# Optimization experiments

Measured on AMD Instinct MI355X. Metric: run time of the kernel, lower is better.

Reference implementation:

```python
import jax, jax.numpy as jnp
import numpy as np

SMALL_CONST = 1e-8
K = 128
N = 512 * 512  # pixels


def setup_inputs() -> dict:
    key = jax.random.key(0)
    ks = jax.random.split(key, 6)
    pos = jax.random.uniform(ks[0], (N, 2), jnp.float32, 0.0, 512.0)      # pixel coords
    mu = jax.random.uniform(ks[1], (K, 2), jnp.float32, 0.0, 512.0)       # gaussian centers
    alpha = jax.random.uniform(ks[2], (K,), jnp.float32)                   # opacities in [0,1]
    color = jax.random.uniform(ks[3], (K, 3), jnp.float32, 0.0, 255.0)     # RGB in [0,255]
    scales = 10.0 + jax.random.uniform(ks[4], (K, 2), jnp.float32) * 20.0  # anisotropic scales
    thetas = jax.random.uniform(ks[5], (K,), jnp.float32, -np.pi, np.pi)   # rotations
    return dict(pos=pos, mu=mu, alpha=alpha, color=color, scales=scales, thetas=thetas)


def _forward(pos, mu, alpha, color, scales, thetas):
    # Parameter clamps done at the top of the torch forward
    alpha = jnp.clip(alpha, 0.0, 1.0)
    color = jnp.clip(color, 0.0, 255.0)
    scales = jnp.clip(scales, 0.1, None)

    # Precompute all K inverse covariances: sigma_inv = R diag(1/s^2) R^T  -> [K,2,2]
    c, s = jnp.cos(thetas), jnp.sin(thetas)
    R = jnp.stack([jnp.stack([c, -s], -1), jnp.stack([s, c], -1)], -2)  # [K,2,2]
    inv2 = 1.0 / scales ** 2                                            # [K,2]
    sigma_inv = jnp.einsum('kti,ki,kji->ktj', R, inv2, R)               # [K,2,2]

    n = pos.shape[0]
    pc0 = jnp.zeros((n, 3), pos.dtype)
    pa0 = jnp.zeros((n, 1), pos.dtype)

    def step(carry, g):
        pc, pa = carry
        mu_k, si_k, a_k, col_k = g
        diff = pos - mu_k                                          # [N,2]
        expo = -0.5 * jnp.einsum('ni,ij,nj->n', diff, si_k, diff)  # [N]
        alpha_k = (a_k * jnp.exp(expo))[:, None]                   # [N,1]
        new_alpha = pa + alpha_k * (1.0 - pa)
        pc = (pc * pa + col_k * alpha_k * (1.0 - pa)) / (new_alpha + SMALL_CONST)
        pc = jnp.clip(pc, 0.0, 255.0)
        pa = jnp.clip(new_alpha, 0.0, 1.0)
        return (pc, pa), None

    (pc, pa), _ = jax.lax.scan(jax.checkpoint(step), (pc0, pa0),
                               (mu, sigma_inv, alpha, color))
    # include_opc=True path: append alpha channel scaled to [0,255]
    return jnp.concatenate([pc, pa * 255.0], axis=-1)  # [N,4]


def reference(pos, mu, alpha, color, scales, thetas):
    return _forward(pos, mu, alpha, color, scales, thetas)
```

## Files before the change

### kernel.cpp

```cpp
#include <hip/hip_runtime.h>
#include <math.h>

#define KG 128
#define CH 8
#define NCHUNK (KG / CH)

typedef float f32x2 __attribute__((ext_vector_type(2)));

__global__ __launch_bounds__(128) void precompute_params(
    const float* __restrict__ mu,
    const float* __restrict__ alpha,
    const float* __restrict__ color,
    const float* __restrict__ scales,
    const float* __restrict__ thetas,
    float4* __restrict__ P0,
    float4* __restrict__ P1,
    float*  __restrict__ P2)
{
    const int k = threadIdx.x;
    if (k >= KG) return;
    const float mx = mu[2 * k];
    const float my = mu[2 * k + 1];
    const float al = fminf(fmaxf(alpha[k], 0.0f), 1.0f);
    const float cr = fminf(fmaxf(color[3 * k + 0], 0.0f), 255.0f);
    const float cg = fminf(fmaxf(color[3 * k + 1], 0.0f), 255.0f);
    const float cb = fminf(fmaxf(color[3 * k + 2], 0.0f), 255.0f);
    const float sx = fmaxf(scales[2 * k + 0], 0.1f);
    const float sy = fmaxf(scales[2 * k + 1], 0.1f);
    const float th = thetas[k];
    const float c = cosf(th);
    const float s = sinf(th);
    const float i0 = 1.0f / (sx * sx);
    const float i1 = 1.0f / (sy * sy);
    const float a  = c * c * i0 + s * s * i1;
    const float b  = c * s * (i0 - i1);
    const float cc = s * s * i0 + c * c * i1;
    const float f = -0.5f * 1.4426950408889634f;
    P0[k] = make_float4(mx, my, a * f, 2.0f * b * f);
    P1[k] = make_float4(cc * f, al, cr, cg);
    P2[k] = cb;
}

__global__ __launch_bounds__(256, 2) void splat_fwd(
    const float* __restrict__ pos,
    const float4* __restrict__ P0,
    const float4* __restrict__ P1,
    const float*  __restrict__ P2,
    float* __restrict__ out,
    int nPairs)
{
    const int t = blockIdx.x * blockDim.x + threadIdx.x;
    if (t >= nPairs) return;

    const float4 pp = reinterpret_cast<const float4*>(pos)[t];
    const f32x2 px = { pp.x, pp.z };
    const f32x2 py = { pp.y, pp.w };

    f32x2 omp   = { 1.0f, 1.0f };
    f32x2 pa    = { 0.0f, 0.0f };
    f32x2 hprev = { 0.0f, 0.0f };
    f32x2 rlast = { 0.0f, 0.0f };
    f32x2 numr  = { 0.0f, 0.0f };
    f32x2 numg  = { 0.0f, 0.0f };
    f32x2 numb  = { 0.0f, 0.0f };

    for (int c = 0; c < NCHUNK; ++c) {
        const int base = c * CH;

        float4 q0[CH], q1[CH];
        float  q2[CH];
#pragma unroll
        for (int j = 0; j < CH; ++j) {
            q0[j] = P0[base + j];
            q1[j] = P1[base + j];
            q2[j] = P2[base + j];
        }

        f32x2 w[CH];
#pragma unroll
        for (int j = 0; j < CH; ++j) {
            const f32x2 dx = px - q0[j].x;
            const f32x2 dy = py - q0[j].y;
            const f32x2 u  = q0[j].z * dx + q0[j].w * dy;
            const f32x2 e  = dx * u + (q1[j].x * dy) * dy;
            f32x2 E;
            E.x = __builtin_amdgcn_exp2f(e.x);
            E.y = __builtin_amdgcn_exp2f(e.y);
            w[j] = q1[j].y * E;
        }

        f32x2 t1[CH], paA[CH];
#pragma unroll
        for (int j = 0; j < CH; ++j) {
            t1[j] = w[j] * omp;
            omp   = omp - w[j] * omp;
            pa    = pa + t1[j];
            paA[j] = pa;
        }

        f32x2 r[CH];
#pragma unroll
        for (int j = 0; j < CH; ++j) {
            const f32x2 nae = paA[j] + 1e-8f;
            r[j].x = __builtin_amdgcn_rcpf(nae.x);
            r[j].y = __builtin_amdgcn_rcpf(nae.y);
        }

#pragma unroll
        for (int j = 0; j < CH; ++j) {
            numr = numr * hprev + q1[j].z * t1[j];
            numg = numg * hprev + q1[j].w * t1[j];
            numb = numb * hprev + q2[j]   * t1[j];
            hprev = paA[j] * r[j];
        }
        rlast = r[CH - 1];
    }

    const f32x2 pcr = numr * rlast;
    const f32x2 pcg = numg * rlast;
    const f32x2 pcb = numb * rlast;

    float4 o0, o1;
    o0.x = fminf(fmaxf(pcr.x, 0.0f), 255.0f);
    o0.y = fminf(fmaxf(pcg.x, 0.0f), 255.0f);
    o0.z = fminf(fmaxf(pcb.x, 0.0f), 255.0f);
    o0.w = fminf(pa.x, 1.0f) * 255.0f;
    o1.x = fminf(fmaxf(pcr.y, 0.0f), 255.0f);
    o1.y = fminf(fmaxf(pcg.y, 0.0f), 255.0f);
    o1.z = fminf(fmaxf(pcb.y, 0.0f), 255.0f);
    o1.w = fminf(pa.y, 1.0f) * 255.0f;

    float4* o = reinterpret_cast<float4*>(out);
    o[2 * t]     = o0;
    o[2 * t + 1] = o1;
}

extern "C" void kernel_launch(void* const* d_in, const int* in_sizes, int n_in,
                              void* d_out, int out_size, void* d_ws, size_t ws_size,
                              hipStream_t stream) {
    const float* pos    = (const float*)d_in[0];
    const float* mu     = (const float*)d_in[1];
    const float* alpha  = (const float*)d_in[2];
    const float* color  = (const float*)d_in[3];
    const float* scales = (const float*)d_in[4];
    const float* thetas = (const float*)d_in[5];
    float* out = (float*)d_out;

    float4* P0 = (float4*)d_ws;
    float4* P1 = P0 + KG;
    float*  P2 = (float*)(P1 + KG);

    const int n = in_sizes[0] / 2;
    const int nPairs = n / 2;
    const int block = 256;
    const int grid = (nPairs + block - 1) / block;

    hipLaunchKernelGGL(precompute_params, dim3(1), dim3(128), 0, stream,
                       mu, alpha, color, scales, thetas, P0, P1, P2);
    hipLaunchKernelGGL(splat_fwd, dim3(grid), dim3(block), 0, stream,
                       pos, P0, P1, P2, out, nPairs);
}
```

Measured before the change: 83.44 us.

## Process one pixel per thread with scalar math and smaller gaussian chunks

Drops the two-pixels-per-thread packed f32x2 formulation in favor of one pixel per thread with explicit fmaf scalar arithmetic, doubling the grid size. The chunk size shrinks from 8 to 4 and launch bounds raise the occupancy hint from 2 to 4 blocks per SIMD/CU. The aim is more waves for latency hiding and lower register pressure, but it gives up packed-FP32 VALU throughput and doubles the per-pixel redundant parameter loads.

```diff
diff --git a/kernel.cpp b/kernel.cpp
--- a/kernel.cpp
+++ b/kernel.cpp
@@ -2,10 +2,8 @@
 #include <math.h>
 
 #define KG 128
-#define CH 8
+#define CH 4
 #define NCHUNK (KG / CH)
-
-typedef float f32x2 __attribute__((ext_vector_type(2)));
 
 __global__ __launch_bounds__(128) void precompute_params(
     const float* __restrict__ mu,
@@ -41,28 +39,25 @@
     P2[k] = cb;
 }
 
-__global__ __launch_bounds__(256, 2) void splat_fwd(
+__global__ __launch_bounds__(256, 4) void splat_fwd(
     const float* __restrict__ pos,
     const float4* __restrict__ P0,
     const float4* __restrict__ P1,
     const float*  __restrict__ P2,
     float* __restrict__ out,
-    int nPairs)
+    int n)
 {
-    const int t = blockIdx.x * blockDim.x + threadIdx.x;
-    if (t >= nPairs) return;
+    const int i = blockIdx.x * blockDim.x + threadIdx.x;
+    if (i >= n) return;
 
-    const float4 pp = reinterpret_cast<const float4*>(pos)[t];
-    const f32x2 px = { pp.x, pp.z };
-    const f32x2 py = { pp.y, pp.w };
+    const float2 p = reinterpret_cast<const float2*>(pos)[i];
+    const float px = p.x, py = p.y;
 
-    f32x2 omp   = { 1.0f, 1.0f };
-    f32x2 pa    = { 0.0f, 0.0f };
-    f32x2 hprev = { 0.0f, 0.0f };
-    f32x2 rlast = { 0.0f, 0.0f };
-    f32x2 numr  = { 0.0f, 0.0f };
-    f32x2 numg  = { 0.0f, 0.0f };
-    f32x2 numb  = { 0.0f, 0.0f };
+    float omp   = 1.0f;
+    float pa    = 0.0f;
+    float hprev = 0.0f;
+    float rlast = 0.0f;
+    float numr = 0.0f, numg = 0.0f, numb = 0.0f;
 
     for (int c = 0; c < NCHUNK; ++c) {
         const int base = c * CH;
@@ -76,63 +71,46 @@
             q2[j] = P2[base + j];
         }
 
-        f32x2 w[CH];
+        float w[CH];
 #pragma unroll
         for (int j = 0; j < CH; ++j) {
-            const f32x2 dx = px - q0[j].x;
-            const f32x2 dy = py - q0[j].y;
-            const f32x2 u  = q0[j].z * dx + q0[j].w * dy;
-            const f32x2 e  = dx * u + (q1[j].x * dy) * dy;
-            f32x2 E;
-            E.x = __builtin_amdgcn_exp2f(e.x);
-            E.y = __builtin_amdgcn_exp2f(e.y);
-            w[j] = q1[j].y * E;
+            const float dx = px - q0[j].x;
+            const float dy = py - q0[j].y;
+            const float u  = fmaf(q0[j].z, dx, q0[j].w * dy);
+            const float e  = fmaf(dx, u, (q1[j].x * dy) * dy);
+            w[j] = q1[j].y * __builtin_amdgcn_exp2f(e);
         }
 
-        f32x2 t1[CH], paA[CH];
+        float t1[CH], paA[CH];
 #pragma unroll
         for (int j = 0; j < CH; ++j) {
             t1[j] = w[j] * omp;
-            omp   = omp - w[j] * omp;
+            omp   = fmaf(-w[j], omp, omp);
             pa    = pa + t1[j];
             paA[j] = pa;
         }
 
-        f32x2 r[CH];
+        float r[CH];
 #pragma unroll
-        for (int j = 0; j < CH; ++j) {
-            const f32x2 nae = paA[j] + 1e-8f;
-            r[j].x = __builtin_amdgcn_rcpf(nae.x);
-            r[j].y = __builtin_amdgcn_rcpf(nae.y);
-        }
+        for (int j = 0; j < CH; ++j)
+            r[j] = __builtin_amdgcn_rcpf(paA[j] + 1e-8f);
 
 #pragma unroll
         for (int j = 0; j < CH; ++j) {
-            numr = numr * hprev + q1[j].z * t1[j];
-            numg = numg * hprev + q1[j].w * t1[j];
-            numb = numb * hprev + q2[j]   * t1[j];
+            numr = fmaf(numr, hprev, q1[j].z * t1[j]);
+            numg = fmaf(numg, hprev, q1[j].w * t1[j]);
+            numb = fmaf(numb, hprev, q2[j]   * t1[j]);
             hprev = paA[j] * r[j];
         }
         rlast = r[CH - 1];
     }
 
-    const f32x2 pcr = numr * rlast;
-    const f32x2 pcg = numg * rlast;
-    const f32x2 pcb = numb * rlast;
-
-    float4 o0, o1;
-    o0.x = fminf(fmaxf(pcr.x, 0.0f), 255.0f);
-    o0.y = fminf(fmaxf(pcg.x, 0.0f), 255.0f);
-    o0.z = fminf(fmaxf(pcb.x, 0.0f), 255.0f);
-    o0.w = fminf(pa.x, 1.0f) * 255.0f;
-    o1.x = fminf(fmaxf(pcr.y, 0.0f), 255.0f);
-    o1.y = fminf(fmaxf(pcg.y, 0.0f), 255.0f);
-    o1.z = fminf(fmaxf(pcb.y, 0.0f), 255.0f);
-    o1.w = fminf(pa.y, 1.0f) * 255.0f;
-
-    float4* o = reinterpret_cast<float4*>(out);
-    o[2 * t]     = o0;
-    o[2 * t + 1] = o1;
+    float4 o;
+    o.x = fminf(fmaxf(numr * rlast, 0.0f), 255.0f);
+    o.y = fminf(fmaxf(numg * rlast, 0.0f), 255.0f);
+    o.z = fminf(fmaxf(numb * rlast, 0.0f), 255.0f);
+    o.w = fminf(pa, 1.0f) * 255.0f;
+    reinterpret_cast<float4*>(out)[i] = o;
 }
 
 extern "C" void kernel_launch(void* const* d_in, const int* in_sizes, int n_in,
@@ -151,12 +129,11 @@
     float*  P2 = (float*)(P1 + KG);
 
     const int n = in_sizes[0] / 2;
-    const int nPairs = n / 2;
     const int block = 256;
-    const int grid = (nPairs + block - 1) / block;
+    const int grid = (n + block - 1) / block;
 
     hipLaunchKernelGGL(precompute_params, dim3(1), dim3(128), 0, stream,
                        mu, alpha, color, scales, thetas, P0, P1, P2);
     hipLaunchKernelGGL(splat_fwd, dim3(grid), dim3(block), 0, stream,
-                       pos, P0, P1, P2, out, nPairs);
+                       pos, P0, P1, P2, out, n);
 }
```

Result: slower. 86.28 us (+3.4%).

## Fuse parameter precompute into splat kernel via shared memory and fold alpha into exponent

Applied to the files above, without the earlier changes.

Removes the separate precompute launch. Each block now recomputes the 128 Gaussian parameters into LDS and reads them from shared memory instead of global memory. The opacity multiply is folded into the exp2 argument as log2(alpha), which saves one multiply per Gaussian. The chunk size is halved from 8 to 4. In exchange, every block redundantly computes sin/cos per Gaussian, a __syncthreads is added, and log2(0) gives -inf, which still yields zero weight.

```diff
diff --git a/kernel.cpp b/kernel.cpp
--- a/kernel.cpp
+++ b/kernel.cpp
@@ -2,54 +2,53 @@
 #include <math.h>
 
 #define KG 128
-#define CH 8
+#define CH 4
 #define NCHUNK (KG / CH)
 
 typedef float f32x2 __attribute__((ext_vector_type(2)));
 
-__global__ __launch_bounds__(128) void precompute_params(
+__global__ __launch_bounds__(256, 2) void splat_fwd(
+    const float* __restrict__ pos,
     const float* __restrict__ mu,
     const float* __restrict__ alpha,
     const float* __restrict__ color,
     const float* __restrict__ scales,
     const float* __restrict__ thetas,
-    float4* __restrict__ P0,
-    float4* __restrict__ P1,
-    float*  __restrict__ P2)
-{
-    const int k = threadIdx.x;
-    if (k >= KG) return;
-    const float mx = mu[2 * k];
-    const float my = mu[2 * k + 1];
-    const float al = fminf(fmaxf(alpha[k], 0.0f), 1.0f);
-    const float cr = fminf(fmaxf(color[3 * k + 0], 0.0f), 255.0f);
-    const float cg = fminf(fmaxf(color[3 * k + 1], 0.0f), 255.0f);
-    const float cb = fminf(fmaxf(color[3 * k + 2], 0.0f), 255.0f);
-    const float sx = fmaxf(scales[2 * k + 0], 0.1f);
-    const float sy = fmaxf(scales[2 * k + 1], 0.1f);
-    const float th = thetas[k];
-    const float c = cosf(th);
-    const float s = sinf(th);
-    const float i0 = 1.0f / (sx * sx);
-    const float i1 = 1.0f / (sy * sy);
-    const float a  = c * c * i0 + s * s * i1;
-    const float b  = c * s * (i0 - i1);
-    const float cc = s * s * i0 + c * c * i1;
-    const float f = -0.5f * 1.4426950408889634f;
-    P0[k] = make_float4(mx, my, a * f, 2.0f * b * f);
-    P1[k] = make_float4(cc * f, al, cr, cg);
-    P2[k] = cb;
-}
-
-__global__ __launch_bounds__(256, 2) void splat_fwd(
-    const float* __restrict__ pos,
-    const float4* __restrict__ P0,
-    const float4* __restrict__ P1,
-    const float*  __restrict__ P2,
     float* __restrict__ out,
     int nPairs)
 {
-    const int t = blockIdx.x * blockDim.x + threadIdx.x;
+    __shared__ float4 sP0[KG];
+    __shared__ float4 sP1[KG];
+    __shared__ float  sP2[KG];
+
+    const int tid = threadIdx.x;
+    if (tid < KG) {
+        const int k = tid;
+        const float mx = mu[2 * k];
+        const float my = mu[2 * k + 1];
+        const float al = fminf(fmaxf(alpha[k], 0.0f), 1.0f);
+        const float cr = fminf(fmaxf(color[3 * k + 0], 0.0f), 255.0f);
+        const float cg = fminf(fmaxf(color[3 * k + 1], 0.0f), 255.0f);
+        const float cb = fminf(fmaxf(color[3 * k + 2], 0.0f), 255.0f);
+        const float sx = fmaxf(scales[2 * k + 0], 0.1f);
+        const float sy = fmaxf(scales[2 * k + 1], 0.1f);
+        const float th = thetas[k];
+        const float c = cosf(th);
+        const float s = sinf(th);
+        const float i0 = 1.0f / (sx * sx);
+        const float i1 = 1.0f / (sy * sy);
+        const float a  = c * c * i0 + s * s * i1;
+        const float b  = c * s * (i0 - i1);
+        const float cc = s * s * i0 + c * c * i1;
+        const float f = -0.5f * 1.4426950408889634f;
+        const float lal = __log2f(al);
+        sP0[k] = make_float4(mx, my, a * f, 2.0f * b * f);
+        sP1[k] = make_float4(cc * f, lal, cr, cg);
+        sP2[k] = cb;
+    }
+    __syncthreads();
+
+    const int t = blockIdx.x * blockDim.x + tid;
     if (t >= nPairs) return;
 
     const float4 pp = reinterpret_cast<const float4*>(pos)[t];
@@ -71,9 +70,9 @@
         float  q2[CH];
 #pragma unroll
         for (int j = 0; j < CH; ++j) {
-            q0[j] = P0[base + j];
-            q1[j] = P1[base + j];
-            q2[j] = P2[base + j];
+            q0[j] = sP0[base + j];
+            q1[j] = sP1[base + j];
+            q2[j] = sP2[base + j];
         }
 
         f32x2 w[CH];
@@ -82,11 +81,10 @@
             const f32x2 dx = px - q0[j].x;
             const f32x2 dy = py - q0[j].y;
             const f32x2 u  = q0[j].z * dx + q0[j].w * dy;
-            const f32x2 e  = dx * u + (q1[j].x * dy) * dy;
-            f32x2 E;
-            E.x = __builtin_amdgcn_exp2f(e.x);
-            E.y = __builtin_amdgcn_exp2f(e.y);
-            w[j] = q1[j].y * E;
+            const f32x2 v  = (q1[j].x * dy) * dy + q1[j].y;
+            const f32x2 e  = dx * u + v;
+            w[j].x = __builtin_amdgcn_exp2f(e.x);
+            w[j].y = __builtin_amdgcn_exp2f(e.y);
         }
 
         f32x2 t1[CH], paA[CH];
@@ -146,17 +144,11 @@
     const float* thetas = (const float*)d_in[5];
     float* out = (float*)d_out;
 
-    float4* P0 = (float4*)d_ws;
-    float4* P1 = P0 + KG;
-    float*  P2 = (float*)(P1 + KG);
-
     const int n = in_sizes[0] / 2;
     const int nPairs = n / 2;
     const int block = 256;
     const int grid = (nPairs + block - 1) / block;
 
-    hipLaunchKernelGGL(precompute_params, dim3(1), dim3(128), 0, stream,
-                       mu, alpha, color, scales, thetas, P0, P1, P2);
     hipLaunchKernelGGL(splat_fwd, dim3(grid), dim3(block), 0, stream,
-                       pos, P0, P1, P2, out, nPairs);
+                       pos, mu, alpha, color, scales, thetas, out, nPairs);
 }
```

After: 81.15 us. 1.03x faster.
